# Performance work log

Measured on AMD Instinct MI355X. Metric: run time of the kernel, lower is better.

Reference implementation:

```python
import jax, jax.numpy as jnp
import numpy as np

N = 8192          # batch size (anchors == candidates, self-mining)
D = 128           # embedding dim
NUM_CLASSES = 256 # label vocabulary
MAX_K = 64        # static cap on negatives sampled per row (k ~= class_count-1 ~ 31)
MIN_DIST = 0.1
MAX_DIST = 1.42


def setup_inputs() -> dict:
    key = jax.random.key(0)
    k1, k2 = jax.random.split(key)
    l_embeds = jax.random.normal(k1, (N, D), dtype=jnp.float32)
    l_labels = jax.random.randint(k2, (N,), 0, NUM_CLASSES)
    return {"l_embeds": l_embeds, "l_labels": l_labels}


def reference(l_embeds, l_labels):
    # --- Miner.forward: L2-normalize embeddings (normalize_embeds=True) ---
    x = l_embeds / jnp.linalg.norm(l_embeds, axis=1, keepdims=True)

    # --- cdist(x, x, p=2) via gram matrix ---
    sq = jnp.sum(x * x, axis=1)                      # [N]
    d2 = sq[:, None] + sq[None, :] - 2.0 * (x @ x.T)  # [N, N]
    dist = jnp.sqrt(jnp.clip(d2, 0.0))

    # Exclude self-pairs: original adds inf on the diagonal; setting the diagonal
    # to MAX_DIST achieves the intended effect (zero weight via dist < max_dist)
    # without inf/nan propagation through log_weights.
    eye = jnp.eye(N, dtype=bool)
    dist = jnp.where(eye, MAX_DIST, dist)
    dist = jnp.clip(dist, MIN_DIST)

    neg = (l_labels[:, None] != l_labels[None, :]).astype(x.dtype)  # [N, N]

    # Distance-weighted sampling weights (inverse of q(d) on the hypersphere)
    d = float(D)
    log_weights = -((d - 2.0) * jnp.log(dist) + (d - 3.0) / 2.0 * (1.0 - dist * dist / 4.0))
    w = jnp.exp(log_weights - jnp.max(log_weights, axis=1, keepdims=True))
    w = w * neg * (dist < MAX_DIST).astype(x.dtype)
    w = w / jnp.clip(jnp.sum(w, axis=1, keepdims=True), 1e-6)  # row-normalized probs

    # Per-row number of negatives to sample: (# same-label rows) - 1 (self)
    counts = jnp.bincount(l_labels, length=NUM_CLASSES)
    k = counts[l_labels] - 1                                    # [N]

    # Vectorized weighted sampling WITH replacement (matches np.random.choice default):
    # categorical over log-probs, MAX_K draws per row, validity-masked to k draws.
    logits = jnp.where(w > 0, jnp.log(w), -1e30)
    keys = jax.random.split(jax.random.key(42), N)
    samples = jax.vmap(lambda kk, lg: jax.random.categorical(kk, lg, shape=(MAX_K,)))(keys, logits)  # [N, MAX_K]
    valid = jnp.arange(MAX_K)[None, :] < k[:, None]             # [N, MAX_K]
    rows = jnp.broadcast_to(jnp.arange(N)[:, None], (N, MAX_K))
    neg_mask = jnp.zeros((N, N), dtype=bool).at[rows, samples].max(valid)

    # Positive mask: same label, excluding self
    pos_mask = (l_labels[:, None] == l_labels[None, :]) & ~eye

    # Original returns nonzero() of pos_mask[:, :, None] & neg_mask[:, None, :]
    # (data-dependent shape); we return the dense masks + sampling weights,
    # from which the triplet index lists are trivially derived.
    return w, pos_mask, neg_mask
```

## Files before the change

kernel.cpp:

```cpp
#include <hip/hip_runtime.h>
#include <stdint.h>
#include <math.h>

#define NROWS 8192
#define DIM   128

__device__ __forceinline__ uint32_t rotl32(uint32_t x, int r) {
  return __builtin_amdgcn_alignbit(x, x, 32 - r);
}

__device__ __forceinline__ void threefry2x32(uint32_t k0, uint32_t k1,
                                             uint32_t x0, uint32_t x1,
                                             uint32_t& o0, uint32_t& o1) {
  uint32_t k2 = k0 ^ k1 ^ 0x1BD11BDAu;
  x0 += k0; x1 += k1;
#define TF4(a,b,c,d) \
  x0 += x1; x1 = rotl32(x1,a); x1 ^= x0; \
  x0 += x1; x1 = rotl32(x1,b); x1 ^= x0; \
  x0 += x1; x1 = rotl32(x1,c); x1 ^= x0; \
  x0 += x1; x1 = rotl32(x1,d); x1 ^= x0;
  TF4(13,15,26,6)
  x0 += k1; x1 += k2 + 1u;
  TF4(17,29,16,24)
  x0 += k2; x1 += k0 + 2u;
  TF4(13,15,26,6)
  x0 += k0; x1 += k1 + 3u;
  TF4(17,29,16,24)
  x0 += k1; x1 += k2 + 4u;
  TF4(13,15,26,6)
  x0 += k2; x1 += k0 + 5u;
#undef TF4
  o0 = x0; o1 = x1;
}

__global__ __launch_bounds__(256) void k_norm(const float* __restrict__ emb,
                                              float* __restrict__ xn,
                                              float* __restrict__ sq) {
  int row  = blockIdx.x * 4 + (threadIdx.x >> 6);
  int lane = threadIdx.x & 63;
  const float* r = emb + (size_t)row * DIM;
  float e0 = r[lane], e1 = r[lane + 64];
  float s = e0 * e0 + e1 * e1;
#pragma unroll
  for (int off = 32; off; off >>= 1) s += __shfl_xor(s, off);
  float nrm = sqrtf(s);
  float x0 = e0 / nrm, x1 = e1 / nrm;
  xn[(size_t)row * DIM + lane]      = x0;
  xn[(size_t)row * DIM + 64 + lane] = x1;
  float s2 = x0 * x0 + x1 * x1;
#pragma unroll
  for (int off = 32; off; off >>= 1) s2 += __shfl_xor(s2, off);
  if (lane == 0) sq[row] = s2;
}

__global__ void k_zero_counts(int* counts) { counts[threadIdx.x] = 0; }

__global__ void k_bincount(const int* __restrict__ lab, int* counts) {
  int i = blockIdx.x * blockDim.x + threadIdx.x;
  atomicAdd(&counts[lab[i]], 1);
}

__global__ void k_prep_rows(const int* __restrict__ lab, const int* __restrict__ counts,
                            int* __restrict__ kk, uint2* __restrict__ keys) {
  int i = blockIdx.x * blockDim.x + threadIdx.x;
  kk[i] = counts[lab[i]] - 1;
  uint32_t o0, o1;
  threefry2x32(0u, 42u, 0u, (uint32_t)i, o0, o1);
  keys[i] = make_uint2(o0, o1);
}

#define LSTR 68

__device__ __forceinline__ void tile_dots(const float* __restrict__ xn, int bi, int bj,
                                          float acc[4][4], float* As, float* Bs) {
  const int tid = threadIdx.x;
  const int ty = tid >> 4, tx = tid & 15;
#pragma unroll
  for (int r = 0; r < 4; ++r)
#pragma unroll
    for (int c = 0; c < 4; ++c) acc[r][c] = 0.0f;

  const int srow   = tid >> 4;
  const int schunk = tid & 15;
  for (int ks = 0; ks < DIM; ks += 64) {
    __syncthreads();
#pragma unroll
    for (int pr = 0; pr < 4; ++pr) {
      int rr = srow + pr * 16;
      float4 a4 = *(const float4*)(xn + (size_t)(bi * 64 + rr) * DIM + ks + schunk * 4);
      float4 b4 = *(const float4*)(xn + (size_t)(bj * 64 + rr) * DIM + ks + schunk * 4);
      int k0 = schunk * 4;
      As[(k0 + 0) * LSTR + rr] = a4.x; As[(k0 + 1) * LSTR + rr] = a4.y;
      As[(k0 + 2) * LSTR + rr] = a4.z; As[(k0 + 3) * LSTR + rr] = a4.w;
      Bs[(k0 + 0) * LSTR + rr] = b4.x; Bs[(k0 + 1) * LSTR + rr] = b4.y;
      Bs[(k0 + 2) * LSTR + rr] = b4.z; Bs[(k0 + 3) * LSTR + rr] = b4.w;
    }
    __syncthreads();
#pragma unroll 8
    for (int k = 0; k < 64; ++k) {
      float4 av = *(const float4*)(As + k * LSTR + ty * 4);
      float4 bv = *(const float4*)(Bs + k * LSTR + tx * 4);
      float a_[4] = {av.x, av.y, av.z, av.w};
      float b_[4] = {bv.x, bv.y, bv.z, bv.w};
#pragma unroll
      for (int r = 0; r < 4; ++r)
#pragma unroll
        for (int c = 0; c < 4; ++c)
          acc[r][c] = fmaf(a_[r], b_[c], acc[r][c]);
    }
  }
}

__global__ __launch_bounds__(256) void k_pass2(const float* __restrict__ xn,
                                               const float* __restrict__ sq,
                                               const int* __restrict__ lab,
                                               float* __restrict__ wout) {
  __shared__ float As[64 * LSTR];
  __shared__ float Bs[64 * LSTR];
  const int bi = blockIdx.y, bj = blockIdx.x;
  float acc[4][4];
  tile_dots(xn, bi, bj, acc, As, Bs);
  const int tid = threadIdx.x, ty = tid >> 4, tx = tid & 15;
  const int gi0 = bi * 64 + ty * 4, gj0 = bj * 64 + tx * 4;
  float sqi[4], sqj[4];
  int li[4], lj[4];
#pragma unroll
  for (int r = 0; r < 4; ++r) { sqi[r] = sq[gi0 + r]; li[r] = lab[gi0 + r]; }
#pragma unroll
  for (int c = 0; c < 4; ++c) { sqj[c] = sq[gj0 + c]; lj[c] = lab[gj0 + c]; }
#pragma unroll
  for (int r = 0; r < 4; ++r) {
    float tmp[4];
#pragma unroll
    for (int c = 0; c < 4; ++c) {
      float d2 = sqi[r] + sqj[c] - 2.0f * acc[r][c];
      float dist = sqrtf(fmaxf(d2, 0.0f));
      if (gi0 + r == gj0 + c) dist = 1.42f;
      dist = fmaxf(dist, 0.1f);
      float wun = 0.0f;
      if ((li[r] != lj[c]) && (dist < 1.42f)) {
        float logw = -(126.0f * logf(dist) + 62.5f * (1.0f - dist * dist * 0.25f));
        wun = expf(logw);
      }
      tmp[c] = wun;
    }
    float4 wv = {tmp[0], tmp[1], tmp[2], tmp[3]};
    *(float4*)(wout + (size_t)(gi0 + r) * NROWS + gj0) = wv;
  }
}

__global__ __launch_bounds__(256) void k_rowsum(const float* __restrict__ w,
                                                float* __restrict__ rowsum) {
  __shared__ float buf[4];
  int i = blockIdx.x, tid = threadIdx.x;
  const float* wr = w + (size_t)i * NROWS;
  float s = 0.0f;
  for (int c = tid; c < NROWS; c += 256) s += wr[c];
#pragma unroll
  for (int off = 32; off; off >>= 1) s += __shfl_xor(s, off);
  if ((tid & 63) == 0) buf[tid >> 6] = s;
  __syncthreads();
  if (tid == 0) rowsum[i] = (buf[0] + buf[1]) + (buf[2] + buf[3]);
}

__global__ __launch_bounds__(256) void k_pass3(const float* __restrict__ rowsum,
                                               const int* __restrict__ lab,
                                               float* __restrict__ w,
                                               float* __restrict__ pos,
                                               float* __restrict__ neg) {
  size_t t = (size_t)blockIdx.x * blockDim.x + threadIdx.x;
  size_t base = t * 4;
  int i = (int)(base >> 13);
  int j = (int)(base & 8191);
  float s = rowsum[i];
  float4 wv = *(float4*)(w + base);
  wv.x /= s; wv.y /= s; wv.z /= s; wv.w /= s;
  *(float4*)(w + base) = wv;
  int li = lab[i];
  int4 lj = *(const int4*)(lab + j);
  float4 pv;
  pv.x = (li == lj.x && (j + 0) != i) ? 1.0f : 0.0f;
  pv.y = (li == lj.y && (j + 1) != i) ? 1.0f : 0.0f;
  pv.z = (li == lj.z && (j + 2) != i) ? 1.0f : 0.0f;
  pv.w = (li == lj.w && (j + 3) != i) ? 1.0f : 0.0f;
  *(float4*)(pos + base) = pv;
  float4 z = {0.0f, 0.0f, 0.0f, 0.0f};
  *(float4*)(neg + base) = z;
}

#define EPS_LAZY 1e-4f
#define ACAP 6400
#define NBINS 128
#define BININV 1.6f
#define GMAXF 15.95f
#define WGS 512

__global__ __launch_bounds__(WGS, 8) void k_sampler(const float* __restrict__ w,
                                                    const int* __restrict__ kk,
                                                    const uint2* __restrict__ keys,
                                                    float* __restrict__ neg) {
  __shared__ unsigned short act[ACAP + 64];
  __shared__ float lact[ACAP + 64];
  __shared__ int hist[NBINS];
  __shared__ float cmax[NBINS];
  __shared__ float redbuf[8];
  __shared__ int acount;
  const int i = blockIdx.x;
  const int kv = kk[i];
  if (kv <= 0) return;
  const int tid = threadIdx.x;
  const int wave = tid >> 6, lane = tid & 63;
  const float* wrow = w + (size_t)i * NROWS;

  if (tid < NBINS) hist[tid] = 0;
  __syncthreads();

  float lmax = -3.4e38f;
  for (int c = tid; c < NROWS; c += WGS) {
    float wv = wrow[c];
    if (wv > 0.0f) {
      float l = logf(wv);
      lmax = fmaxf(lmax, l);
      int bn = (int)(-l * BININV);
      bn = (bn < 0) ? 0 : ((bn > NBINS - 1) ? NBINS - 1 : bn);
      atomicAdd(&hist[bn], 1);
    }
  }
#pragma unroll
  for (int off = 32; off; off >>= 1) lmax = fmaxf(lmax, __shfl_xor(lmax, off));
  if (lane == 0) redbuf[wave] = lmax;
  __syncthreads();
  float gmax = redbuf[0];
#pragma unroll
  for (int rwv = 1; rwv < 8; ++rwv) gmax = fmaxf(gmax, redbuf[rwv]);
  float T = gmax - 20.43f;
  int bcut = (int)(-T * BININV);
  if (bcut > NBINS - 1) bcut = NBINS - 1;

  if (wave == 0) {
    int ex0 = 0, ex1 = 0, tot = 0;
    for (int k = 0; k < NBINS; ++k) {
      int h = (k <= bcut) ? hist[k] : 0;
      if (k < lane) ex0 += h;
      if (k < lane + 64) ex1 += h;
      tot += h;
    }
    hist[lane] = ex0;
    hist[lane + 64] = ex1;
    if (lane == 0) acount = tot;
  }
  __syncthreads();
  int A = acount;
  if (A > ACAP) A = ACAP;
  if (A == 0) return;

  for (int c = tid; c < NROWS; c += WGS) {
    float wv = wrow[c];
    if (wv > 0.0f) {
      float l = logf(wv);
      int bn = (int)(-l * BININV);
      bn = (bn < 0) ? 0 : ((bn > NBINS - 1) ? NBINS - 1 : bn);
      if (bn <= bcut) {
        int slot = atomicAdd(&hist[bn], 1);
        if (slot < ACAP) {
          act[slot] = (unsigned short)c;
          lact[slot] = l;
        }
      }
    }
  }
  __syncthreads();
  if (tid < 64) { act[A + tid] = 0; lact[A + tid] = -3.4e38f; }
  __syncthreads();
  const int nch = (A + 63) >> 6;
  for (int j = wave; j < nch; j += 8) {
    float v = lact[(j << 6) + lane];
#pragma unroll
    for (int off = 32; off; off >>= 1) v = fmaxf(v, __shfl_xor(v, off));
    if (lane == 0) cmax[j] = v;
  }
  __syncthreads();
  if (wave == 0) {
    float v1 = (lane + 64 < nch) ? cmax[lane + 64] : -3.4e38f;
    float v0 = (lane < nch) ? cmax[lane] : -3.4e38f;
#pragma unroll
    for (int off = 1; off < 64; off <<= 1) {
      float t1 = __shfl_down(v1, off); if (lane < 64 - off) v1 = fmaxf(v1, t1);
      float t0 = __shfl_down(v0, off); if (lane < 64 - off) v0 = fmaxf(v0, t0);
    }
    float h1max = __shfl(v1, 0);
    v0 = fmaxf(v0, h1max);
    if (lane < nch) cmax[lane] = v0;
    if (lane + 64 < nch) cmax[lane + 64] = v1;
  }
  __syncthreads();
  const uint2 key = keys[i];

  for (int t = 0; t < 8; ++t) {
    const int s = wave + 8 * t;
    if (s >= kv) break;
    const uint32_t sbase = (uint32_t)(s * NROWS);
    float sbest = -3.4e38f, sbeps = -3.4e38f;
    int sidx = 0x7FFFFFFF;
    int j = 0;
    for (int base = 0; base < A; base += 64, ++j) {
      if (cmax[j] + GMAXF < sbest) break;
      int a = base + lane;
      int c = act[a];
      float l = lact[a];
      uint32_t r0, r1;
      threefry2x32(key.x, key.y, 0u, sbase + (uint32_t)c, r0, r1);
      uint32_t b = (r0 ^ r1) >> 9;
      float bf = (float)b;
      float e1 = __expf(l - sbeps);
      float thr = fmaf(__expf(-e1), 8388608.0f, -128.0f);
      if (__any(bf > thr)) {
        float u = b ? (bf * 1.1920928955078125e-7f) : 1.1754943508222875e-38f;
        float ge = -logf(-logf(u));
        float ze = l + ge;
        int cc = c;
#pragma unroll
        for (int off = 1; off < 64; off <<= 1) {
          float oz = __shfl_xor(ze, off);
          int oc = __shfl_xor(cc, off);
          if (oz > ze || (oz == ze && oc < cc)) { ze = oz; cc = oc; }
        }
        if (ze > sbest || (ze == sbest && cc < sidx)) {
          sbest = ze; sidx = cc; sbeps = sbest - EPS_LAZY;
        }
      }
    }
    if (lane == 0) {
      neg[(size_t)i * NROWS + sidx] = 1.0f;
    }
  }
}

extern "C" void kernel_launch(void* const* d_in, const int* in_sizes, int n_in,
                              void* d_out, int out_size, void* d_ws, size_t ws_size,
                              hipStream_t stream) {
  const float* emb = (const float*)d_in[0];
  const int* lab   = (const int*)d_in[1];
  float* out = (float*)d_out;
  const size_t NN = (size_t)NROWS * NROWS;
  float* w   = out;
  float* pos = out + NN;
  float* neg = out + 2 * NN;

  char* wsb = (char*)d_ws;
  float* xn     = (float*)(wsb);
  float* sq     = (float*)(wsb + 4194304);
  float* rowsum = (float*)(wsb + 4194304 + 32768);
  int*   kk     = (int*)  (wsb + 4194304 + 65536);
  uint2* keys   = (uint2*)(wsb + 4194304 + 98304);
  int*   counts = (int*)  (wsb + 4194304 + 163840);

  k_norm<<<NROWS / 4, 256, 0, stream>>>(emb, xn, sq);
  k_zero_counts<<<1, 256, 0, stream>>>(counts);
  k_bincount<<<NROWS / 256, 256, 0, stream>>>(lab, counts);
  k_prep_rows<<<NROWS / 256, 256, 0, stream>>>(lab, counts, kk, keys);
  dim3 g(NROWS / 64, NROWS / 64);
  k_pass2<<<g, 256, 0, stream>>>(xn, sq, lab, w);
  k_rowsum<<<NROWS, 256, 0, stream>>>(w, rowsum);
  k_pass3<<<(unsigned)(NN / 1024), 256, 0, stream>>>(rowsum, lab, w, pos, neg);
  k_sampler<<<NROWS, WGS, 0, stream>>>(w, kk, keys, neg);
}
```

Measured before the change: 3.273 ms.

## Fuse row-sum, normalization and mask writes into the sampler kernel

Removes the separate row-sum and normalize/mask kernels and does that work per row inside the sampler block, so the N×N weight matrix is read and written fewer times in global memory. The histogram pass now works on the freshly normalized values in registers. The lazy Gumbel threshold test is rewritten to use the stored weight and a single exp2 per element, with logs taken only when needed. This adds a row-sum and normalize phase at the start of every sampler block, and the sampler's reads of the row now come right after that same block wrote it.

```diff
diff --git a/kernel.cpp b/kernel.cpp
--- a/kernel.cpp
+++ b/kernel.cpp
@@ -149,87 +149,80 @@
   }
 }
 
-__global__ __launch_bounds__(256) void k_rowsum(const float* __restrict__ w,
-                                                float* __restrict__ rowsum) {
-  __shared__ float buf[4];
-  int i = blockIdx.x, tid = threadIdx.x;
-  const float* wr = w + (size_t)i * NROWS;
-  float s = 0.0f;
-  for (int c = tid; c < NROWS; c += 256) s += wr[c];
-#pragma unroll
-  for (int off = 32; off; off >>= 1) s += __shfl_xor(s, off);
-  if ((tid & 63) == 0) buf[tid >> 6] = s;
-  __syncthreads();
-  if (tid == 0) rowsum[i] = (buf[0] + buf[1]) + (buf[2] + buf[3]);
-}
-
-__global__ __launch_bounds__(256) void k_pass3(const float* __restrict__ rowsum,
-                                               const int* __restrict__ lab,
-                                               float* __restrict__ w,
-                                               float* __restrict__ pos,
-                                               float* __restrict__ neg) {
-  size_t t = (size_t)blockIdx.x * blockDim.x + threadIdx.x;
-  size_t base = t * 4;
-  int i = (int)(base >> 13);
-  int j = (int)(base & 8191);
-  float s = rowsum[i];
-  float4 wv = *(float4*)(w + base);
-  wv.x /= s; wv.y /= s; wv.z /= s; wv.w /= s;
-  *(float4*)(w + base) = wv;
-  int li = lab[i];
-  int4 lj = *(const int4*)(lab + j);
-  float4 pv;
-  pv.x = (li == lj.x && (j + 0) != i) ? 1.0f : 0.0f;
-  pv.y = (li == lj.y && (j + 1) != i) ? 1.0f : 0.0f;
-  pv.z = (li == lj.z && (j + 2) != i) ? 1.0f : 0.0f;
-  pv.w = (li == lj.w && (j + 3) != i) ? 1.0f : 0.0f;
-  *(float4*)(pos + base) = pv;
-  float4 z = {0.0f, 0.0f, 0.0f, 0.0f};
-  *(float4*)(neg + base) = z;
-}
-
 #define EPS_LAZY 1e-4f
 #define ACAP 6400
 #define NBINS 128
 #define BININV 1.6f
 #define GMAXF 15.95f
 #define WGS 512
-
-__global__ __launch_bounds__(WGS, 8) void k_sampler(const float* __restrict__ w,
+#define LOG2E 1.4426950408889634f
+
+__global__ __launch_bounds__(WGS, 8) void k_sampler(const int* __restrict__ lab,
                                                     const int* __restrict__ kk,
                                                     const uint2* __restrict__ keys,
+                                                    float* __restrict__ w,
+                                                    float* __restrict__ pos,
                                                     float* __restrict__ neg) {
   __shared__ unsigned short act[ACAP + 64];
-  __shared__ float lact[ACAP + 64];
+  __shared__ float wact[ACAP + 64];
   __shared__ int hist[NBINS];
   __shared__ float cmax[NBINS];
   __shared__ float redbuf[8];
+  __shared__ float sbuf[4];
   __shared__ int acount;
   const int i = blockIdx.x;
+  const int tid = threadIdx.x;
+  const int wave = tid >> 6, lane = tid & 63;
+  float* wrow   = w   + (size_t)i * NROWS;
+  float* posrow = pos + (size_t)i * NROWS;
+  float* negrow = neg + (size_t)i * NROWS;
+
+  if (tid < 256) {
+    float s0 = 0.0f;
+    for (int c = tid; c < NROWS; c += 256) s0 += wrow[c];
+#pragma unroll
+    for (int off = 32; off; off >>= 1) s0 += __shfl_xor(s0, off);
+    if ((tid & 63) == 0) sbuf[tid >> 6] = s0;
+  }
+  if (tid < NBINS) hist[tid] = 0;
+  __syncthreads();
+  const float s = (sbuf[0] + sbuf[1]) + (sbuf[2] + sbuf[3]);
+
+  const int li = lab[i];
+  float lmax = -3.4e38f;
+  for (int c4 = tid * 4; c4 < NROWS; c4 += WGS * 4) {
+    float4 wv = *(float4*)(wrow + c4);
+    wv.x /= s; wv.y /= s; wv.z /= s; wv.w /= s;
+    *(float4*)(wrow + c4) = wv;
+    int4 lj = *(const int4*)(lab + c4);
+    float4 pv;
+    pv.x = (li == lj.x && (c4 + 0) != i) ? 1.0f : 0.0f;
+    pv.y = (li == lj.y && (c4 + 1) != i) ? 1.0f : 0.0f;
+    pv.z = (li == lj.z && (c4 + 2) != i) ? 1.0f : 0.0f;
+    pv.w = (li == lj.w && (c4 + 3) != i) ? 1.0f : 0.0f;
+    *(float4*)(posrow + c4) = pv;
+    float4 z4 = {0.0f, 0.0f, 0.0f, 0.0f};
+    *(float4*)(negrow + c4) = z4;
+    float wa[4] = {wv.x, wv.y, wv.z, wv.w};
+#pragma unroll
+    for (int e = 0; e < 4; ++e) {
+      if (wa[e] > 0.0f) {
+        float l = logf(wa[e]);
+        lmax = fmaxf(lmax, l);
+        int bn = (int)(-l * BININV);
+        bn = (bn < 0) ? 0 : ((bn > NBINS - 1) ? NBINS - 1 : bn);
+        atomicAdd(&hist[bn], 1);
+      }
+    }
+  }
+#pragma unroll
+  for (int off = 32; off; off >>= 1) lmax = fmaxf(lmax, __shfl_xor(lmax, off));
+  if (lane == 0) redbuf[wave] = lmax;
+  __syncthreads();
+
   const int kv = kk[i];
   if (kv <= 0) return;
-  const int tid = threadIdx.x;
-  const int wave = tid >> 6, lane = tid & 63;
-  const float* wrow = w + (size_t)i * NROWS;
-
-  if (tid < NBINS) hist[tid] = 0;
-  __syncthreads();
-
-  float lmax = -3.4e38f;
-  for (int c = tid; c < NROWS; c += WGS) {
-    float wv = wrow[c];
-    if (wv > 0.0f) {
-      float l = logf(wv);
-      lmax = fmaxf(lmax, l);
-      int bn = (int)(-l * BININV);
-      bn = (bn < 0) ? 0 : ((bn > NBINS - 1) ? NBINS - 1 : bn);
-      atomicAdd(&hist[bn], 1);
-    }
-  }
-#pragma unroll
-  for (int off = 32; off; off >>= 1) lmax = fmaxf(lmax, __shfl_xor(lmax, off));
-  if (lane == 0) redbuf[wave] = lmax;
-  __syncthreads();
+
   float gmax = redbuf[0];
 #pragma unroll
   for (int rwv = 1; rwv < 8; ++rwv) gmax = fmaxf(gmax, redbuf[rwv]);
@@ -264,20 +257,20 @@
         int slot = atomicAdd(&hist[bn], 1);
         if (slot < ACAP) {
           act[slot] = (unsigned short)c;
-          lact[slot] = l;
+          wact[slot] = wv;
         }
       }
     }
   }
   __syncthreads();
-  if (tid < 64) { act[A + tid] = 0; lact[A + tid] = -3.4e38f; }
+  if (tid < 64) { act[A + tid] = 0; wact[A + tid] = 0.0f; }
   __syncthreads();
   const int nch = (A + 63) >> 6;
   for (int j = wave; j < nch; j += 8) {
-    float v = lact[(j << 6) + lane];
+    float v = wact[(j << 6) + lane];
 #pragma unroll
     for (int off = 32; off; off >>= 1) v = fmaxf(v, __shfl_xor(v, off));
-    if (lane == 0) cmax[j] = v;
+    if (lane == 0) cmax[j] = logf(v);
   }
   __syncthreads();
   if (wave == 0) {
@@ -297,26 +290,27 @@
   const uint2 key = keys[i];
 
   for (int t = 0; t < 8; ++t) {
-    const int s = wave + 8 * t;
-    if (s >= kv) break;
-    const uint32_t sbase = (uint32_t)(s * NROWS);
-    float sbest = -3.4e38f, sbeps = -3.4e38f;
+    const int sN = wave + 8 * t;
+    if (sN >= kv) break;
+    const uint32_t sbase = (uint32_t)(sN * NROWS);
+    float sbest = -3.4e38f;
+    float nesl = -3.4e38f;
     int sidx = 0x7FFFFFFF;
     int j = 0;
     for (int base = 0; base < A; base += 64, ++j) {
       if (cmax[j] + GMAXF < sbest) break;
       int a = base + lane;
       int c = act[a];
-      float l = lact[a];
+      float wn = wact[a];
       uint32_t r0, r1;
       threefry2x32(key.x, key.y, 0u, sbase + (uint32_t)c, r0, r1);
       uint32_t b = (r0 ^ r1) >> 9;
       float bf = (float)b;
-      float e1 = __expf(l - sbeps);
-      float thr = fmaf(__expf(-e1), 8388608.0f, -128.0f);
+      float thr = fmaf(__builtin_amdgcn_exp2f(wn * nesl), 8388608.0f, -128.0f);
       if (__any(bf > thr)) {
         float u = b ? (bf * 1.1920928955078125e-7f) : 1.1754943508222875e-38f;
         float ge = -logf(-logf(u));
+        float l = logf(wn);
         float ze = l + ge;
         int cc = c;
 #pragma unroll
@@ -326,12 +320,13 @@
           if (oz > ze || (oz == ze && oc < cc)) { ze = oz; cc = oc; }
         }
         if (ze > sbest || (ze == sbest && cc < sidx)) {
-          sbest = ze; sidx = cc; sbeps = sbest - EPS_LAZY;
+          sbest = ze; sidx = cc;
+          nesl = -LOG2E * __expf(EPS_LAZY - sbest);
         }
       }
     }
     if (lane == 0) {
-      neg[(size_t)i * NROWS + sidx] = 1.0f;
+      negrow[sidx] = 1.0f;
     }
   }
 }
@@ -350,7 +345,6 @@
   char* wsb = (char*)d_ws;
   float* xn     = (float*)(wsb);
   float* sq     = (float*)(wsb + 4194304);
-  float* rowsum = (float*)(wsb + 4194304 + 32768);
   int*   kk     = (int*)  (wsb + 4194304 + 65536);
   uint2* keys   = (uint2*)(wsb + 4194304 + 98304);
   int*   counts = (int*)  (wsb + 4194304 + 163840);
@@ -361,7 +355,5 @@
   k_prep_rows<<<NROWS / 256, 256, 0, stream>>>(lab, counts, kk, keys);
   dim3 g(NROWS / 64, NROWS / 64);
   k_pass2<<<g, 256, 0, stream>>>(xn, sq, lab, w);
-  k_rowsum<<<NROWS, 256, 0, stream>>>(w, rowsum);
-  k_pass3<<<(unsigned)(NN / 1024), 256, 0, stream>>>(rowsum, lab, w, pos, neg);
-  k_sampler<<<NROWS, WGS, 0, stream>>>(w, kk, keys, neg);
-}
+  k_sampler<<<NROWS, WGS, 0, stream>>>(lab, kk, keys, w, pos, neg);
+}
```

Result: faster. 3.070 ms (-6.2%).
